# Kernel tuning notes

Hardware: AMD Instinct MI355X
Metric: run time of the kernel (lower is better)

The kernel has to match this reference:

```python
import jax, jax.numpy as jnp
import numpy as np

FEATURE_W = 1.0
TRIPLET_W = 1.0
SOFT_W = 1.0
MARGIN = 0.2
TEMP = 1.0
COMMIT_W = 0.1
DISTORT_W = 0.1
STRIDE = 320

B, T, D, K = 8, 1500, 512, 4096


def setup_inputs() -> dict:
    key = jax.random.key(0)
    k1, k2, k3, k4, k5 = jax.random.split(key, 5)
    return {
        "student_features": jax.random.normal(k1, (B, T, D), dtype=jnp.float32),
        "teacher_features": jax.random.normal(k2, (B, T, D), dtype=jnp.float32),
        "teacher_codes": jax.random.randint(k3, (B, T), 0, K),
        "codebook": jax.random.normal(k4, (K, D), dtype=jnp.float32),
        "lengths": jax.random.randint(k5, (B,), 0, T * STRIDE),
    }


def _sq_dists(flat, codebook):
    x2 = jnp.sum(flat * flat, axis=-1, keepdims=True)          # (N,1)
    c2 = jnp.sum(codebook * codebook, axis=-1)[None, :]        # (1,K)
    xc = jnp.einsum("nd,kd->nk", flat, codebook)               # (N,K)
    return jnp.maximum(x2 + c2 - 2.0 * xc, 0.0)


def reference(student_features, teacher_features, teacher_codes, codebook, lengths):
    b, t, d = student_features.shape
    # valid-frame mask from sample lengths
    valid = jnp.minimum(lengths // STRIDE, t)                  # (B,)
    mask = (jnp.arange(t)[None, :] < valid[:, None]).astype(student_features.dtype)  # (B,T)
    msum = jnp.sum(mask)

    # feature loss: masked mean of per-token MSE
    diff = student_features - teacher_features
    feature_loss = jnp.sum(jnp.mean(diff * diff, axis=-1) * mask) / msum

    # triplet loss
    pos_dist = jnp.sqrt(jnp.sum(diff * diff, axis=-1))
    neg_teacher = jnp.roll(teacher_features, shift=1, axis=0)
    nd = student_features - neg_teacher
    neg_dist = jnp.sqrt(jnp.sum(nd * nd, axis=-1))
    triplet = jax.nn.relu(pos_dist - neg_dist + MARGIN)
    triplet_loss = jnp.sum(triplet * mask) / msum

    # soft token (KL distillation over codebook logits)
    s_flat = student_features.reshape(-1, d)                   # (B*T, D)
    t_flat = teacher_features.reshape(-1, d)
    s_logits = -_sq_dists(s_flat, codebook) / TEMP             # (B*T, K)
    t_logits = -_sq_dists(t_flat, codebook) / TEMP
    s_logp = jax.nn.log_softmax(s_logits, axis=-1)
    t_logp = jax.nn.log_softmax(t_logits, axis=-1)
    t_prob = jax.lax.stop_gradient(jnp.exp(t_logp))
    t_logp = jax.lax.stop_gradient(t_logp)
    kl_per_token = jnp.sum(t_prob * (t_logp - s_logp), axis=-1)  # (B*T,)
    flat_mask = mask.reshape(-1)
    soft_loss = jnp.sum(kl_per_token * flat_mask) / msum

    # VQ commitment / distortion (nearest-code quantization)
    codes = jnp.argmax(s_logits, axis=-1)                       # argmin dist == argmax logits
    quantized = codebook[codes].reshape(b, t, d)
    cdiff = student_features - jax.lax.stop_gradient(quantized)
    commitment_loss = jnp.mean(cdiff * cdiff)
    ddiff = jax.lax.stop_gradient(student_features) - quantized
    distortion_loss = jnp.mean(ddiff * ddiff)

    total = (FEATURE_W * feature_loss + TRIPLET_W * triplet_loss
             + SOFT_W * soft_loss + COMMIT_W * commitment_loss
             + DISTORT_W * distortion_loss)
    return total
```

## Files before the change

kernel.cpp:

```cpp
#include <hip/hip_runtime.h>

typedef unsigned short u16;
typedef unsigned int   u32;
typedef float  f32x16 __attribute__((ext_vector_type(16)));
typedef __bf16 bf16x8 __attribute__((ext_vector_type(8)));

#define B_N   8
#define T_N   1500
#define D_N   512
#define K_N   4096
#define NTOK  12000
#define STRD  320

#define X2S_OFF     0u
#define C2_OFF      49152u
#define FEATP_OFF   65536u
#define TRIPP_OFF   67584u
#define STATEP_OFF  69632u
#define SBF_OFF     1048576u
#define TBF_OFF     (1048576u + 12288000u)
#define CBBF_OFF    (1048576u + 24576000u)

#define ST_S1  12000
#define ST_SQ  48000


__device__ __forceinline__ u16 f2bf(float x){
  u32 u = __float_as_uint(x);
  u32 r = (u + 0x7fffu + ((u >> 16) & 1u)) >> 16;
  return (u16)r;
}

__device__ __forceinline__ void gl_lds16(const void* g, void* l){
  __builtin_amdgcn_global_load_lds(
      (__attribute__((address_space(1))) void*)(g),
      (__attribute__((address_space(3))) void*)(l),
      16, 0, 0);
}

__device__ __forceinline__ void merge_state(float& m, float& Z, float om, float oZ){
  float nm = fmaxf(m, om);
  Z = Z*__expf(m - nm) + oZ*__expf(om - nm);
  m = nm;
}
__device__ __forceinline__ void merge_stateT(float& m, float& Z, float& A,
                                             float om, float oZ, float oA){
  float nm = fmaxf(m, om);
  float e0 = __expf(m - nm), e1 = __expf(om - nm);
  Z = Z*e0 + oZ*e1; A = A*e0 + oA*e1; m = nm;
}

__global__ __launch_bounds__(256) void prep_kernel(
    const float* __restrict__ s, const float* __restrict__ t,
    const float* __restrict__ cb, const int* __restrict__ lengths,
    u16* __restrict__ sbf, u16* __restrict__ tbf, u16* __restrict__ cbbf,
    float* __restrict__ x2s, float* __restrict__ c2,
    float* __restrict__ featP, float* __restrict__ tripP)
{
  const int tid = threadIdx.x;
  const int w = tid >> 6, lane = tid & 63;
  __shared__ float sred[3][32];

  if (blockIdx.x < 375){
    const int tt = blockIdx.x;
    const int t8 = lane >> 3, kpart = lane & 7;
    const int tokL = w*8 + t8;
    const int n = tt*32 + tokL;
    const int b = n / T_N, tok = n - b*T_N;
    const int nr = ((b+7)&7)*T_N + tok;
    const float* srow = s + (size_t)n  * D_N;
    const float* trow = t + (size_t)n  * D_N;
    const float* rrow = t + (size_t)nr * D_N;

    float x2 = 0.f, sd2 = 0.f, nd2 = 0.f;
    uint4 sbq[8], tbq[8];
#pragma unroll
    for (int q = 0; q < 8; ++q){
      const int kl = q*64 + kpart*8;
      float4 a0 = *(const float4*)(srow + kl), a1 = *(const float4*)(srow + kl + 4);
      float4 b0 = *(const float4*)(trow + kl), b1 = *(const float4*)(trow + kl + 4);
      float4 r0 = *(const float4*)(rrow + kl), r1 = *(const float4*)(rrow + kl + 4);
      float sv[8] = {a0.x,a0.y,a0.z,a0.w,a1.x,a1.y,a1.z,a1.w};
      float tv[8] = {b0.x,b0.y,b0.z,b0.w,b1.x,b1.y,b1.z,b1.w};
      float rv[8] = {r0.x,r0.y,r0.z,r0.w,r1.x,r1.y,r1.z,r1.w};
      u16 sb[8], tb[8];
#pragma unroll
      for (int i = 0; i < 8; ++i){
        float d = sv[i] - tv[i]; sd2 += d*d;
        x2 += sv[i]*sv[i];
        float e = sv[i] - rv[i]; nd2 += e*e;
        sb[i] = f2bf(sv[i]); tb[i] = f2bf(tv[i]);
      }
      sbq[q].x = (u32)sb[0] | ((u32)sb[1]<<16); sbq[q].y = (u32)sb[2] | ((u32)sb[3]<<16);
      sbq[q].z = (u32)sb[4] | ((u32)sb[5]<<16); sbq[q].w = (u32)sb[6] | ((u32)sb[7]<<16);
      tbq[q].x = (u32)tb[0] | ((u32)tb[1]<<16); tbq[q].y = (u32)tb[2] | ((u32)tb[3]<<16);
      tbq[q].z = (u32)tb[4] | ((u32)tb[5]<<16); tbq[q].w = (u32)tb[6] | ((u32)tb[7]<<16);
    }
#pragma unroll
    for (int q = 0; q < 8; ++q){
      const int ks = q*4 + (kpart >> 1), kh = kpart & 1;
      const size_t chunk = ((size_t)tt*32 + ks)*64 + kh*32 + tokL;
      ((uint4*)sbf)[chunk] = sbq[q];
      ((uint4*)tbf)[chunk] = tbq[q];
    }
#pragma unroll
    for (int mm = 1; mm < 8; mm <<= 1){
      x2  += __shfl_xor(x2,  mm);
      sd2 += __shfl_xor(sd2, mm);
      nd2 += __shfl_xor(nd2, mm);
    }
    if (kpart == 0){ sred[0][tokL] = x2; sred[1][tokL] = sd2; sred[2][tokL] = nd2; }
    __syncthreads();
    if (tid < 32){
      float X2 = sred[0][tid], SD = sred[1][tid], ND = sred[2][tid];
      int n2 = tt*32 + tid, b2 = n2 / T_N, tk2 = n2 - b2*T_N;
      x2s[n2] = X2;
      int valid = lengths[b2] / STRD; if (valid > T_N) valid = T_N;
      float mf = (tk2 < valid) ? 1.f : 0.f;
      float fp = mf * SD * (1.f/512.f);
      float tp = mf * fmaxf(sqrtf(SD) - sqrtf(ND) + 0.2f, 0.f);
#pragma unroll
      for (int mm = 1; mm < 32; mm <<= 1){ fp += __shfl_xor(fp, mm); tp += __shfl_xor(tp, mm); }
      if (tid == 0){ featP[tt] = fp; tripP[tt] = tp; }
    }
  } else {
    const int idx = blockIdx.x - 375;
    const int ctile = idx*4 + w;
    const int kh = lane >> 5, sp = lane & 31;
    const int ch = ctile >> 5, cg = (ctile >> 3) & 3, ctg = ctile & 7;
    const int code = ctile*32 + sp;
    const float* crow = cb + (size_t)code * D_N;

    float s2 = 0.f;
#pragma unroll
    for (int stp = 0; stp < 32; ++stp){
      const int kc = stp >> 1, ks2 = stp & 1;
      const int k0 = stp*16 + kh*8;
      float4 c0 = *(const float4*)(crow + k0), c1 = *(const float4*)(crow + k0 + 4);
      float cv[8] = {c0.x,c0.y,c0.z,c0.w,c1.x,c1.y,c1.z,c1.w};
      u16 cbv[8];
#pragma unroll
      for (int i = 0; i < 8; ++i){ s2 += cv[i]*cv[i]; cbv[i] = f2bf(cv[i]); }
      uint4 pk;
      pk.x = (u32)cbv[0] | ((u32)cbv[1]<<16); pk.y = (u32)cbv[2] | ((u32)cbv[3]<<16);
      pk.z = (u32)cbv[4] | ((u32)cbv[5]<<16); pk.w = (u32)cbv[6] | ((u32)cbv[7]<<16);
      const size_t off = ((size_t)(ch*64 + cg*16 + kc))*8192 + ctg*1024 + ks2*512 + lane*8;
      *(uint4*)(cbbf + off) = pk;
    }
    s2 += __shfl_xor(s2, 32);
    if (lane < 32) c2[ctile*32 + lane] = s2;
  }
}

__global__ __launch_bounds__(256, 2) void main_kl_kernel(
    const u16* __restrict__ sbf, const u16* __restrict__ tbf,
    const u16* __restrict__ cbbf, const float* __restrict__ c2,
    float* __restrict__ stateP)
{
  __shared__ u16 Ab[32768];

  const int tid = threadIdx.x;
  const int w = tid >> 6, lane = tid & 63;
  const int kh = lane >> 5;
  const int blk = blockIdx.x;
  const int tt = blk % 375, ch = blk / 375;

  const u16* cbB = cbbf + (size_t)ch * 524288;
  const u16* sA = sbf + (size_t)tt * 16384;
  const u16* tA = tbf + (size_t)tt * 16384;

#pragma unroll
  for (int r = 0; r < 8; ++r){
    const int off = (r*256 + tid)*8;
    gl_lds16(sA + off, &Ab[off]);
    gl_lds16(tA + off, &Ab[16384 + off]);
  }

  bf16x8 b00, b01, b10, b11;
  {
    const u16* rg = cbB;
    b00 = *(const bf16x8*)(rg + (w*2+0)*1024 +       lane*8);
    b01 = *(const bf16x8*)(rg + (w*2+0)*1024 + 512 + lane*8);
    b10 = *(const bf16x8*)(rg + (w*2+1)*1024 +       lane*8);
    b11 = *(const bf16x8*)(rg + (w*2+1)*1024 + 512 + lane*8);
  }

  __syncthreads();

  float mS = -3e38f, zS = 0.f, mT = -3e38f, zT = 0.f, aa = 0.f;
  f32x16 a0s, a0t, a1s, a1t;

  for (int c = 0; c < 64; ++c){
    const int kc = c & 15;
    if (kc == 0){
#pragma unroll
      for (int i = 0; i < 16; ++i){ a0s[i]=0.f; a0t[i]=0.f; a1s[i]=0.f; a1t[i]=0.f; }
    }
    bf16x8 n00 = b00, n01 = b01, n10 = b10, n11 = b11;
    if (c < 63){
      const u16* rg = cbB + (size_t)(c+1)*8192;
      n00 = *(const bf16x8*)(rg + (w*2+0)*1024 +       lane*8);
      n01 = *(const bf16x8*)(rg + (w*2+0)*1024 + 512 + lane*8);
      n10 = *(const bf16x8*)(rg + (w*2+1)*1024 +       lane*8);
      n11 = *(const bf16x8*)(rg + (w*2+1)*1024 + 512 + lane*8);
    }

    const u16* ap = &Ab[kc*1024 + lane*8];
    bf16x8 as0 = *(const bf16x8*)(ap);
    bf16x8 as1 = *(const bf16x8*)(ap + 512);
    bf16x8 at0 = *(const bf16x8*)(ap + 16384);
    bf16x8 at1 = *(const bf16x8*)(ap + 16896);

    a0s = __builtin_amdgcn_mfma_f32_32x32x16_bf16(b00, as0, a0s, 0, 0, 0);
    a0t = __builtin_amdgcn_mfma_f32_32x32x16_bf16(b00, at0, a0t, 0, 0, 0);
    a1s = __builtin_amdgcn_mfma_f32_32x32x16_bf16(b10, as0, a1s, 0, 0, 0);
    a1t = __builtin_amdgcn_mfma_f32_32x32x16_bf16(b10, at0, a1t, 0, 0, 0);
    a0s = __builtin_amdgcn_mfma_f32_32x32x16_bf16(b01, as1, a0s, 0, 0, 0);
    a0t = __builtin_amdgcn_mfma_f32_32x32x16_bf16(b01, at1, a0t, 0, 0, 0);
    a1s = __builtin_amdgcn_mfma_f32_32x32x16_bf16(b11, as1, a1s, 0, 0, 0);
    a1t = __builtin_amdgcn_mfma_f32_32x32x16_bf16(b11, at1, a1t, 0, 0, 0);
    b00 = n00; b01 = n01; b10 = n10; b11 = n11;

    if (kc == 15){
      const int cg = c >> 4;
#pragma unroll
      for (int ct = 0; ct < 2; ++ct){
        const f32x16& vS = ct ? a1s : a0s;
        const f32x16& vT = ct ? a1t : a0t;
        const int ctg = w*2 + ct;
        const float* c2b = c2 + ch*1024 + cg*256 + ctg*32 + kh*4;
        float4 g0 = *(const float4*)(c2b);
        float4 g1 = *(const float4*)(c2b + 8);
        float4 g2 = *(const float4*)(c2b + 16);
        float4 g3 = *(const float4*)(c2b + 24);
        float c2v[16] = {g0.x,g0.y,g0.z,g0.w, g1.x,g1.y,g1.z,g1.w,
                         g2.x,g2.y,g2.z,g2.w, g3.x,g3.y,g3.z,g3.w};
        float ms_t = -3e38f, mt_t = -3e38f;
#pragma unroll
        for (int i = 0; i < 16; ++i){
          ms_t = fmaxf(ms_t, 2.0f*vS[i] - c2v[i]);
          mt_t = fmaxf(mt_t, 2.0f*vT[i] - c2v[i]);
        }
        float nmS = fmaxf(mS, ms_t), nmT = fmaxf(mT, mt_t);
        float esS = __expf(mS - nmS), esT = __expf(mT - nmT);
        zS *= esS; zT *= esT; aa *= esT;
#pragma unroll
        for (int i = 0; i < 16; ++i){
          float sl = 2.0f*vS[i] - c2v[i];
          float tl = 2.0f*vT[i] - c2v[i];
          zS += __expf(sl - nmS);
          float e = __expf(tl - nmT);
          zT += e; aa += e*(tl - sl);
        }
        mS = nmS; mT = nmT;
      }
    }
  }

  {
    float om = __shfl_xor(mS, 32), oZ = __shfl_xor(zS, 32);
    merge_state(mS, zS, om, oZ);
    float omt = __shfl_xor(mT, 32), ozt = __shfl_xor(zT, 32), oA = __shfl_xor(aa, 32);
    merge_stateT(mT, zT, aa, omt, ozt, oA);
  }
  __syncthreads();
  float* wst = (float*)&Ab[0];
  if (lane < 32){
    float* pw = wst + (w*32 + lane)*5;
    pw[0] = mS; pw[1] = zS; pw[2] = mT; pw[3] = zT; pw[4] = aa;
  }
  __syncthreads();
  if (tid < 32){
    const float* p0 = wst + tid*5;
    float m_s = p0[0], z_s = p0[1], m_t = p0[2], z_t = p0[3], a = p0[4];
#pragma unroll
    for (int ww = 1; ww < 4; ++ww){
      const float* pw = wst + (ww*32 + tid)*5;
      merge_state(m_s, z_s, pw[0], pw[1]);
      merge_stateT(m_t, z_t, a, pw[2], pw[3], pw[4]);
    }
    const int n = tt*32 + tid;
    stateP[0*ST_SQ + ch*ST_S1 + n] = m_s;
    stateP[1*ST_SQ + ch*ST_S1 + n] = z_s;
    stateP[2*ST_SQ + ch*ST_S1 + n] = m_t;
    stateP[3*ST_SQ + ch*ST_S1 + n] = z_t;
    stateP[4*ST_SQ + ch*ST_S1 + n] = a;
  }
}

__global__ __launch_bounds__(1024) void tail_kernel(
    const float* __restrict__ stateP, const float* __restrict__ x2s,
    const float* __restrict__ featP, const float* __restrict__ tripP,
    const int* __restrict__ lengths, float* __restrict__ out)
{
  const int tid = threadIdx.x;
  double kl_s = 0.0, md_s = 0.0, f = 0.0, tr = 0.0;
  for (int n = tid; n < NTOK; n += 1024){
    float m_s = stateP[0*ST_SQ + n], z_s = stateP[1*ST_SQ + n];
    float m_t = stateP[2*ST_SQ + n], z_t = stateP[3*ST_SQ + n], a = stateP[4*ST_SQ + n];
#pragma unroll
    for (int chh = 1; chh < 4; ++chh){
      merge_state(m_s, z_s, stateP[0*ST_SQ + chh*ST_S1 + n], stateP[1*ST_SQ + chh*ST_S1 + n]);
      merge_stateT(m_t, z_t, a, stateP[2*ST_SQ + chh*ST_S1 + n],
                   stateP[3*ST_SQ + chh*ST_S1 + n], stateP[4*ST_SQ + chh*ST_S1 + n]);
    }
    float klv = a / z_t - (m_t + __logf(z_t)) + (m_s + __logf(z_s));
    int b = n / T_N, tk = n - b*T_N;
    int valid = lengths[b] / STRD; if (valid > T_N) valid = T_N;
    if (tk < valid) kl_s += (double)klv;
    md_s += (double)fmaxf(x2s[n] - m_s, 0.f);
  }
  for (int i = tid; i < 375; i += 1024){ f += (double)featP[i]; tr += (double)tripP[i]; }
#pragma unroll
  for (int mm = 1; mm < 64; mm <<= 1){
    kl_s += __shfl_xor(kl_s, mm); md_s += __shfl_xor(md_s, mm);
    f    += __shfl_xor(f,    mm); tr   += __shfl_xor(tr,   mm);
  }
  __shared__ double red[16][4];
  const int w = tid >> 6, lane = tid & 63;
  if (lane == 0){ red[w][0]=kl_s; red[w][1]=md_s; red[w][2]=f; red[w][3]=tr; }
  __syncthreads();
  if (tid == 0){
    double KL=0, MD=0, F=0, TR=0;
    for (int ww = 0; ww < 16; ++ww){ KL+=red[ww][0]; MD+=red[ww][1]; F+=red[ww][2]; TR+=red[ww][3]; }
    long msum = 0;
    for (int b = 0; b < 8; ++b){ int v = lengths[b] / STRD; if (v > T_N) v = T_N; msum += v; }
    double inv = 1.0 / (double)msum;
    double total = F*inv + TR*inv + KL*inv + 0.2 * MD / ((double)B_N * T_N * D_N);
    out[0] = (float)total;
  }
}

extern "C" void kernel_launch(void* const* d_in, const int* in_sizes, int n_in,
                              void* d_out, int out_size, void* d_ws, size_t ws_size,
                              hipStream_t stream)
{
  const float* s  = (const float*)d_in[0];
  const float* t  = (const float*)d_in[1];
  const float* cb = (const float*)d_in[3];
  const int* lengths = (const int*)d_in[4];

  char* ws = (char*)d_ws;
  float* x2s    = (float*)(ws + X2S_OFF);
  float* c2     = (float*)(ws + C2_OFF);
  float* featP  = (float*)(ws + FEATP_OFF);
  float* tripP  = (float*)(ws + TRIPP_OFF);
  float* stateP = (float*)(ws + STATEP_OFF);
  u16* sbf  = (u16*)(ws + SBF_OFF);
  u16* tbf  = (u16*)(ws + TBF_OFF);
  u16* cbbf = (u16*)(ws + CBBF_OFF);

  prep_kernel<<<407, 256, 0, stream>>>(s, t, cb, lengths, sbf, tbf, cbbf,
                                       x2s, c2, featP, tripP);
  main_kl_kernel<<<1500, 256, 0, stream>>>(sbf, tbf, cbbf, c2, stateP);
  tail_kernel<<<1, 1024, 0, stream>>>(stateP, x2s, featP, tripP, lengths, (float*)d_out);
}
```

Measured before the change: 237.1 us.

## Pack student and teacher tokens into one MFMA tile, halve per-block token tile

```diff
diff --git a/kernel.cpp b/kernel.cpp
--- a/kernel.cpp
+++ b/kernel.cpp
@@ -152,28 +152,32 @@
   }
 }
 
-__global__ __launch_bounds__(256, 2) void main_kl_kernel(
+__global__ __launch_bounds__(256, 4) void main_kl_kernel(
     const u16* __restrict__ sbf, const u16* __restrict__ tbf,
     const u16* __restrict__ cbbf, const float* __restrict__ c2,
     float* __restrict__ stateP)
 {
-  __shared__ u16 Ab[32768];
+  __shared__ u16 Ab[16384];
 
   const int tid = threadIdx.x;
   const int w = tid >> 6, lane = tid & 63;
   const int kh = lane >> 5;
   const int blk = blockIdx.x;
-  const int tt = blk % 375, ch = blk / 375;
+  const int tt16 = blk % 750, ch = blk / 750;
+  const int tt32 = tt16 >> 1, half = tt16 & 1;
 
   const u16* cbB = cbbf + (size_t)ch * 524288;
-  const u16* sA = sbf + (size_t)tt * 16384;
-  const u16* tA = tbf + (size_t)tt * 16384;
-
-#pragma unroll
-  for (int r = 0; r < 8; ++r){
-    const int off = (r*256 + tid)*8;
-    gl_lds16(sA + off, &Ab[off]);
-    gl_lds16(tA + off, &Ab[16384 + off]);
+
+  {
+    const int mat  = (lane >> 4) & 1;
+    const int tok4 = lane & 15;
+    const u16* abase = mat ? tbf : sbf;
+    const size_t srcb = (size_t)(tt32*32)*64 + kh*32 + half*16 + tok4;
+#pragma unroll
+    for (int r = 0; r < 8; ++r){
+      const int ks = r*4 + w;
+      gl_lds16(abase + (srcb + (size_t)ks*64)*8, &Ab[ks*512 + lane*8]);
+    }
   }
 
   bf16x8 b00, b01, b10, b11;
@@ -187,14 +191,14 @@
 
   __syncthreads();
 
-  float mS = -3e38f, zS = 0.f, mT = -3e38f, zT = 0.f, aa = 0.f;
-  f32x16 a0s, a0t, a1s, a1t;
+  float mL = -3e38f, zL = 0.f, aL = 0.f;
+  f32x16 a0, a1;
 
   for (int c = 0; c < 64; ++c){
     const int kc = c & 15;
     if (kc == 0){
 #pragma unroll
-      for (int i = 0; i < 16; ++i){ a0s[i]=0.f; a0t[i]=0.f; a1s[i]=0.f; a1t[i]=0.f; }
+      for (int i = 0; i < 16; ++i){ a0[i] = 0.f; a1[i] = 0.f; }
     }
     bf16x8 n00 = b00, n01 = b01, n10 = b10, n11 = b11;
     if (c < 63){
@@ -208,25 +212,18 @@
     const u16* ap = &Ab[kc*1024 + lane*8];
     bf16x8 as0 = *(const bf16x8*)(ap);
     bf16x8 as1 = *(const bf16x8*)(ap + 512);
-    bf16x8 at0 = *(const bf16x8*)(ap + 16384);
-    bf16x8 at1 = *(const bf16x8*)(ap + 16896);
-
-    a0s = __builtin_amdgcn_mfma_f32_32x32x16_bf16(b00, as0, a0s, 0, 0, 0);
-    a0t = __builtin_amdgcn_mfma_f32_32x32x16_bf16(b00, at0, a0t, 0, 0, 0);
-    a1s = __builtin_amdgcn_mfma_f32_32x32x16_bf16(b10, as0, a1s, 0, 0, 0);
-    a1t = __builtin_amdgcn_mfma_f32_32x32x16_bf16(b10, at0, a1t, 0, 0, 0);
-    a0s = __builtin_amdgcn_mfma_f32_32x32x16_bf16(b01, as1, a0s, 0, 0, 0);
-    a0t = __builtin_amdgcn_mfma_f32_32x32x16_bf16(b01, at1, a0t, 0, 0, 0);
-    a1s = __builtin_amdgcn_mfma_f32_32x32x16_bf16(b11, as1, a1s, 0, 0, 0);
-    a1t = __builtin_amdgcn_mfma_f32_32x32x16_bf16(b11, at1, a1t, 0, 0, 0);
+
+    a0 = __builtin_amdgcn_mfma_f32_32x32x16_bf16(b00, as0, a0, 0, 0, 0);
+    a1 = __builtin_amdgcn_mfma_f32_32x32x16_bf16(b10, as0, a1, 0, 0, 0);
+    a0 = __builtin_amdgcn_mfma_f32_32x32x16_bf16(b01, as1, a0, 0, 0, 0);
+    a1 = __builtin_amdgcn_mfma_f32_32x32x16_bf16(b11, as1, a1, 0, 0, 0);
     b00 = n00; b01 = n01; b10 = n10; b11 = n11;
 
     if (kc == 15){
       const int cg = c >> 4;
 #pragma unroll
       for (int ct = 0; ct < 2; ++ct){
-        const f32x16& vS = ct ? a1s : a0s;
-        const f32x16& vT = ct ? a1t : a0t;
+        const f32x16& v = ct ? a1 : a0;
         const int ctg = w*2 + ct;
         const float* c2b = c2 + ch*1024 + cg*256 + ctg*32 + kh*4;
         float4 g0 = *(const float4*)(c2b);
@@ -235,56 +232,53 @@
         float4 g3 = *(const float4*)(c2b + 24);
         float c2v[16] = {g0.x,g0.y,g0.z,g0.w, g1.x,g1.y,g1.z,g1.w,
                          g2.x,g2.y,g2.z,g2.w, g3.x,g3.y,g3.z,g3.w};
-        float ms_t = -3e38f, mt_t = -3e38f;
+        float mloc = -3e38f;
+#pragma unroll
+        for (int i = 0; i < 16; ++i) mloc = fmaxf(mloc, 2.0f*v[i] - c2v[i]);
+        float nm = fmaxf(mL, mloc);
+        float e0 = __expf(mL - nm);
+        zL *= e0; aL *= e0;
 #pragma unroll
         for (int i = 0; i < 16; ++i){
-          ms_t = fmaxf(ms_t, 2.0f*vS[i] - c2v[i]);
-          mt_t = fmaxf(mt_t, 2.0f*vT[i] - c2v[i]);
+          float lv = 2.0f*v[i] - c2v[i];
+          float ov = __shfl_xor(lv, 16);
+          float e = __expf(lv - nm);
+          zL += e; aL += e*(lv - ov);
         }
-        float nmS = fmaxf(mS, ms_t), nmT = fmaxf(mT, mt_t);
-        float esS = __expf(mS - nmS), esT = __expf(mT - nmT);
-        zS *= esS; zT *= esT; aa *= esT;
-#pragma unroll
-        for (int i = 0; i < 16; ++i){
-          float sl = 2.0f*vS[i] - c2v[i];
-          float tl = 2.0f*vT[i] - c2v[i];
-          zS += __expf(sl - nmS);
-          float e = __expf(tl - nmT);
-          zT += e; aa += e*(tl - sl);
-        }
-        mS = nmS; mT = nmT;
+        mL = nm;
       }
     }
   }
 
   {
-    float om = __shfl_xor(mS, 32), oZ = __shfl_xor(zS, 32);
-    merge_state(mS, zS, om, oZ);
-    float omt = __shfl_xor(mT, 32), ozt = __shfl_xor(zT, 32), oA = __shfl_xor(aa, 32);
-    merge_stateT(mT, zT, aa, omt, ozt, oA);
+    float om = __shfl_xor(mL, 32), oz = __shfl_xor(zL, 32), oa = __shfl_xor(aL, 32);
+    merge_stateT(mL, zL, aL, om, oz, oa);
   }
   __syncthreads();
   float* wst = (float*)&Ab[0];
   if (lane < 32){
-    float* pw = wst + (w*32 + lane)*5;
-    pw[0] = mS; pw[1] = zS; pw[2] = mT; pw[3] = zT; pw[4] = aa;
+    float* pw = wst + (w*32 + lane)*3;
+    pw[0] = mL; pw[1] = zL; pw[2] = aL;
   }
   __syncthreads();
   if (tid < 32){
-    const float* p0 = wst + tid*5;
-    float m_s = p0[0], z_s = p0[1], m_t = p0[2], z_t = p0[3], a = p0[4];
+    const float* p0 = wst + tid*3;
+    float m = p0[0], z = p0[1], a = p0[2];
 #pragma unroll
     for (int ww = 1; ww < 4; ++ww){
-      const float* pw = wst + (ww*32 + tid)*5;
-      merge_state(m_s, z_s, pw[0], pw[1]);
-      merge_stateT(m_t, z_t, a, pw[2], pw[3], pw[4]);
-    }
-    const int n = tt*32 + tid;
-    stateP[0*ST_SQ + ch*ST_S1 + n] = m_s;
-    stateP[1*ST_SQ + ch*ST_S1 + n] = z_s;
-    stateP[2*ST_SQ + ch*ST_S1 + n] = m_t;
-    stateP[3*ST_SQ + ch*ST_S1 + n] = z_t;
-    stateP[4*ST_SQ + ch*ST_S1 + n] = a;
+      const float* pw = wst + (ww*32 + tid)*3;
+      merge_stateT(m, z, a, pw[0], pw[1], pw[2]);
+    }
+    const int mat = tid >> 4, tok4 = tid & 15;
+    const int n = tt16*16 + tok4;
+    if (mat == 0){
+      stateP[0*ST_SQ + ch*ST_S1 + n] = m;
+      stateP[1*ST_SQ + ch*ST_S1 + n] = z;
+    } else {
+      stateP[2*ST_SQ + ch*ST_S1 + n] = m;
+      stateP[3*ST_SQ + ch*ST_S1 + n] = z;
+      stateP[4*ST_SQ + ch*ST_S1 + n] = a;
+    }
   }
 }
 
@@ -352,6 +346,6 @@
 
   prep_kernel<<<407, 256, 0, stream>>>(s, t, cb, lengths, sbf, tbf, cbbf,
                                        x2s, c2, featP, tripP);
-  main_kl_kernel<<<1500, 256, 0, stream>>>(sbf, tbf, cbbf, c2, stateP);
+  main_kl_kernel<<<3000, 256, 0, stream>>>(sbf, tbf, cbbf, c2, stateP);
   tail_kernel<<<1, 1024, 0, stream>>>(stateP, x2s, featP, tripP, lengths, (float*)d_out);
 }
```

Result: slower. 273.4 us (+15.3%).
